# Optimization experiments

Hardware: AMD Instinct MI355X
Metric: run time of the kernel (lower is better)

## Reference

```python
import jax, jax.numpy as jnp
import numpy as np

C = 512
NUM_GROUPS = 32
EPS = 1e-6


def setup_inputs() -> dict:
    key = jax.random.key(0)
    ks = jax.random.split(key, 6)
    B, H, W = 4, 64, 64
    x = jax.random.normal(ks[0], (B, H, W, C), dtype=jnp.float32)
    # GroupNorm affine params (flax default init: scale=1, bias=0)
    gn_scale = jnp.ones((C,), jnp.float32)
    gn_bias = jnp.zeros((C,), jnp.float32)
    # 1x1 convs == per-pixel dense layers; weight [C_in, C_out], bias [C_out]
    def dense(k):
        return jax.random.normal(k, (C, C), dtype=jnp.float32) * 0.02
    wq, wk, wv, wo = dense(ks[1]), dense(ks[2]), dense(ks[3]), dense(ks[4])
    bq = jnp.zeros((C,), jnp.float32)
    bk = jnp.zeros((C,), jnp.float32)
    bv = jnp.zeros((C,), jnp.float32)
    bo = jnp.zeros((C,), jnp.float32)
    return {"x": x, "gn_scale": gn_scale, "gn_bias": gn_bias,
            "wq": wq, "bq": bq, "wk": wk, "bk": bk,
            "wv": wv, "bv": bv, "wo": wo, "bo": bo}


def _group_norm(x, scale, bias):
    B, H, W, Cc = x.shape
    g = NUM_GROUPS
    xg = x.reshape(B, H, W, g, Cc // g)
    mean = jnp.mean(xg, axis=(1, 2, 4), keepdims=True)
    var = jnp.var(xg, axis=(1, 2, 4), keepdims=True)
    xn = (xg - mean) * jax.lax.rsqrt(var + EPS)
    xn = xn.reshape(B, H, W, Cc)
    return xn * scale + bias


def reference(x, gn_scale, gn_bias, wq, bq, wk, bk, wv, bv, wo, bo):
    B, H, W, Cc = x.shape
    hn = _group_norm(x, gn_scale, gn_bias)
    # 1x1 convs
    q = (hn @ wq + bq).reshape(B, H * W, Cc)
    k = (hn @ wk + bk).reshape(B, H * W, Cc)
    v = (hn @ wv + bv).reshape(B, H * W, Cc)
    scale = jnp.asarray(Cc, x.dtype) ** -0.5
    # scores[b,i,j] = <q_i, k_j> * c^-0.5; softmax over keys j
    attn = jax.nn.softmax(jnp.einsum('bic,bjc->bij', q, k) * scale, axis=-1)
    out = jnp.einsum('bij,bjc->bic', attn, v).reshape(B, H, W, Cc)
    return x + (out @ wo + bo)
```

## Files before the change

kernel.cpp:

```cpp
#include <hip/hip_runtime.h>


typedef __attribute__((ext_vector_type(8))) __bf16 bf16x8;
typedef __attribute__((ext_vector_type(4))) __bf16 bf16x4;
typedef __attribute__((ext_vector_type(4))) float  floatx4;

#define C_DIM 512
#define SPB   4096
#define MTOT  16384

#define HN_OFF  ((size_t)0)
#define Q_OFF   ((size_t)16 << 20)
#define K_OFF   ((size_t)32 << 20)
#define V4_OFF  ((size_t)48 << 20)
#define WT_OFF  ((size_t)64 << 20)
#define O1_OFF  ((size_t)68 << 20)
#define ML_OFF  ((size_t)84 << 20)
#define GS_OFF  (ML_OFF + (size_t)(256 << 10))

__device__ inline floatx4 mfma16(bf16x8 a, bf16x8 b, floatx4 c) {
    return __builtin_amdgcn_mfma_f32_16x16x32_bf16(a, b, c, 0, 0, 0);
}

__device__ inline void gload16(const void* g, void* lds) {
    __builtin_amdgcn_global_load_lds(
        (const __attribute__((address_space(1))) unsigned int*)g,
        (__attribute__((address_space(3))) unsigned int*)lds, 16, 0, 0);
}

__global__ __launch_bounds__(256) void zero_stats(float* gstats) {
    gstats[threadIdx.x] = 0.f;
}

__global__ __launch_bounds__(256) void gn_stats(
    const float* __restrict__ x, float* __restrict__ gstats) {
    int bg = blockIdx.x;
    int b = bg >> 5, g = bg & 31;
    int tid = threadIdx.x;
    int cq = tid & 3, s0 = tid >> 2;
    const float* base = x + (size_t)b * SPB * C_DIM + g * 16 + cq * 4
                          + (size_t)blockIdx.y * 1024 * C_DIM;
    float sum = 0.f, sq = 0.f;
#pragma unroll 4
    for (int i = 0; i < 16; ++i) {
        floatx4 v = *(const floatx4*)(base + (size_t)(i * 64 + s0) * C_DIM);
        sum += v[0] + v[1] + v[2] + v[3];
        sq  += v[0]*v[0] + v[1]*v[1] + v[2]*v[2] + v[3]*v[3];
    }
#pragma unroll
    for (int off = 1; off < 64; off <<= 1) {
        sum += __shfl_xor(sum, off);
        sq  += __shfl_xor(sq,  off);
    }
    __shared__ float sm[8];
    int w = tid >> 6, lane = tid & 63;
    if (lane == 0) { sm[w] = sum; sm[4 + w] = sq; }
    __syncthreads();
    if (tid == 0) {
        atomicAdd(&gstats[bg * 2],     sm[0] + sm[1] + sm[2] + sm[3]);
        atomicAdd(&gstats[bg * 2 + 1], sm[4] + sm[5] + sm[6] + sm[7]);
    }
}

__global__ __launch_bounds__(256) void gn_apply(
    const float* __restrict__ x, const float* __restrict__ gstats,
    const float* __restrict__ gsc, const float* __restrict__ gbi,
    __bf16* __restrict__ hn) {
    int bg = blockIdx.x;
    int b = bg >> 5, g = bg & 31;
    int tid = threadIdx.x;
    int cq = tid & 3, s0 = tid >> 2;
    float S  = gstats[bg * 2], Qs = gstats[bg * 2 + 1];
    float mean = S * (1.f / 65536.f);
    float var  = Qs * (1.f / 65536.f) - mean * mean;
    float rstd = rsqrtf(var + 1e-6f);
    float sc[4], bi[4];
#pragma unroll
    for (int j = 0; j < 4; ++j) {
        float s_ = gsc[g * 16 + cq * 4 + j] * rstd;
        sc[j] = s_;
        bi[j] = gbi[g * 16 + cq * 4 + j] - mean * s_;
    }
    size_t off = (size_t)b * SPB * C_DIM + g * 16 + cq * 4
               + (size_t)blockIdx.y * 1024 * C_DIM;
    const float* base = x + off;
    __bf16* hbase = hn + off;
#pragma unroll 4
    for (int i = 0; i < 16; ++i) {
        floatx4 v = *(const floatx4*)(base + (size_t)(i * 64 + s0) * C_DIM);
        bf16x4 o;
#pragma unroll
        for (int j = 0; j < 4; ++j) o[j] = (__bf16)(v[j] * sc[j] + bi[j]);
        *(bf16x4*)(hbase + (size_t)(i * 64 + s0) * C_DIM) = o;
    }
}

__global__ __launch_bounds__(256) void wt_kernel(
    const float* __restrict__ w0, const float* __restrict__ w1,
    const float* __restrict__ w2, const float* __restrict__ w3,
    __bf16* __restrict__ wt) {
    const float* srcs[4] = {w0, w1, w2, w3};
    const float* src = srcs[blockIdx.z];
    __bf16* dst = wt + (size_t)blockIdx.z * C_DIM * C_DIM;
    __shared__ float tile[32][33];
    int tx = threadIdx.x & 31, ty = threadIdx.x >> 5;
    int gx = blockIdx.x * 32, gy = blockIdx.y * 32;
#pragma unroll
    for (int i = 0; i < 4; ++i)
        tile[ty + i * 8][tx] = src[(size_t)(gy + ty + i * 8) * C_DIM + gx + tx];
    __syncthreads();
#pragma unroll
    for (int i = 0; i < 4; ++i) {
        int n = gx + ty + i * 8;
        int k = gy + tx;
        dst[(size_t)n * C_DIM + k] = (__bf16)tile[tx][ty + i * 8];
    }
}

__global__ __launch_bounds__(256, 2) void proj_qkv(
    const __bf16* __restrict__ hn, const __bf16* __restrict__ wt_all,
    const float* __restrict__ bq, const float* __restrict__ bk,
    const float* __restrict__ bv, __bf16* __restrict__ qout,
    __bf16* __restrict__ kout, __bf16* __restrict__ v4out) {
    int z = blockIdx.z;
    const __bf16* wt = wt_all + (size_t)z * C_DIM * C_DIM;
    const float* bias = (z == 0) ? bq : (z == 1) ? bk : bv;
    __shared__ __bf16 Alds[128 * 32];
    __shared__ __bf16 Blds[128 * 32];
    int tid = threadIdx.x, lane = tid & 63, w = tid >> 6;
    int c = lane & 15, quad = lane >> 4;
    int wm = w & 1, wn = w >> 1;
    int mbase = blockIdx.x * 128, nbase = blockIdx.y * 128;
    floatx4 acc[4][4] = {};
    for (int kb = 0; kb < 16; ++kb) {
        __syncthreads();
#pragma unroll
        for (int p = 0; p < 2; ++p) {
            int chunk0 = w * 128 + p * 64;
            int chunk = chunk0 + lane;
            int row = chunk >> 2, qk = chunk & 3;
            gload16(hn + (size_t)(mbase + row) * C_DIM + kb * 32 + qk * 8, Alds + chunk0 * 8);
            gload16(wt + (size_t)(nbase + row) * C_DIM + kb * 32 + qk * 8, Blds + chunk0 * 8);
        }
        __syncthreads();
        bf16x8 af[4], bfr[4];
#pragma unroll
        for (int mt = 0; mt < 4; ++mt)
            af[mt] = *(const bf16x8*)(Alds + (wm * 64 + mt * 16 + c) * 32 + quad * 8);
#pragma unroll
        for (int nt = 0; nt < 4; ++nt)
            bfr[nt] = *(const bf16x8*)(Blds + (wn * 64 + nt * 16 + c) * 32 + quad * 8);
#pragma unroll
        for (int mt = 0; mt < 4; ++mt)
#pragma unroll
            for (int nt = 0; nt < 4; ++nt)
                acc[mt][nt] = mfma16(af[mt], bfr[nt], acc[mt][nt]);
    }
    float scale = (z == 0) ? 0.0441941738241592f : 1.0f;
#pragma unroll
    for (int nt = 0; nt < 4; ++nt) {
        int n = nbase + wn * 64 + nt * 16 + c;
        float bval = bias[n];
#pragma unroll
        for (int mt = 0; mt < 4; ++mt) {
            int m0 = mbase + wm * 64 + mt * 16 + quad * 4;
#pragma unroll
            for (int r = 0; r < 4; ++r) {
                int m = m0 + r;
                float val = (acc[mt][nt][r] + bval) * scale;
                if (z == 0)      qout[(size_t)m * C_DIM + n] = (__bf16)val;
                else if (z == 1) kout[(size_t)m * C_DIM + n] = (__bf16)val;
                else {
                    int bb = m >> 12, pos = m & 4095;
                    v4out[((size_t)(bb * 512 + (pos >> 3)) * C_DIM + n) * 8 + (pos & 7)] = (__bf16)val;
                }
            }
        }
    }
}

__device__ inline void stage_K(const __bf16* kbase, int key0,
                               __bf16* Klds, int w, int lane) {
#pragma unroll
    for (int p = 0; p < 8; ++p) {
        int chunk0 = w * 512 + p * 64;
        int chunk = chunk0 + lane;
        gload16(kbase + (size_t)(key0 + (chunk & 31)) * C_DIM + (chunk >> 5) * 8,
                Klds + chunk0 * 8);
    }
}

__global__ __launch_bounds__(256, 2) void flash_kernel(
    const __bf16* __restrict__ q, const __bf16* __restrict__ kmat,
    const __bf16* __restrict__ v4, __bf16* __restrict__ op0,
    __bf16* __restrict__ op1, float* __restrict__ lpart) {
    __shared__ __bf16 Klds[16384];
    __shared__ __bf16 Plds[64 * 40];
    int tid = threadIdx.x, lane = tid & 63, w = tid >> 6;
    int c = lane & 15, quad = lane >> 4;
    int bid = blockIdx.x;
    int xcd = bid & 7;
    int b = xcd >> 1, h = xcd & 1, qt = bid >> 3;

    const __bf16* qp = q + ((size_t)(b * SPB + qt * 64 + w * 16 + c)) * C_DIM + quad * 8;
    bf16x8 qf[16];
#pragma unroll
    for (int ks = 0; ks < 16; ++ks) qf[ks] = *(const bf16x8*)(qp + ks * 32);
    floatx4 o[4][8];
#pragma unroll
    for (int mg = 0; mg < 4; ++mg)
#pragma unroll
        for (int t = 0; t < 8; ++t) o[mg][t] = (floatx4){0.f, 0.f, 0.f, 0.f};
    float l_r[4] = {0.f, 0.f, 0.f, 0.f};

    const __bf16* kbase = kmat + (size_t)b * SPB * C_DIM;
    const __bf16* vbase = v4 + (size_t)b * 512 * C_DIM * 8;

    stage_K(kbase, h * 2048, Klds, w, lane);
    __syncthreads();

    for (int kt = 0; kt < 64; ++kt) {
        int key0 = h * 2048 + kt * 32;
        const __bf16* vp = vbase
            + ((size_t)((key0 >> 3) + quad) * C_DIM + w * 128 + c) * 8;
        bf16x8 vreg[8];
#pragma unroll
        for (int t = 0; t < 8; ++t)
            vreg[t] = *(const bf16x8*)(vp + (size_t)t * 16 * 8);
        floatx4 s0 = (floatx4){0.f,0.f,0.f,0.f}, s1 = (floatx4){0.f,0.f,0.f,0.f};
#pragma unroll
        for (int ks = 0; ks < 16; ++ks) {
            bf16x8 k0 = *(const bf16x8*)(Klds + (((ks * 4 + quad) * 32) + c) * 8);
            bf16x8 k1 = *(const bf16x8*)(Klds + (((ks * 4 + quad) * 32) + c + 16) * 8);
            s0 = mfma16(qf[ks], k0, s0);
            s1 = mfma16(qf[ks], k1, s1);
        }
#pragma unroll
        for (int r = 0; r < 4; ++r) {
            float p0 = __expf(s0[r]);
            float p1 = __expf(s1[r]);
            l_r[r] += p0 + p1;
            int row = w * 16 + quad * 4 + r;
            Plds[row * 40 + c]      = (__bf16)p0;
            Plds[row * 40 + c + 16] = (__bf16)p1;
        }
        __syncthreads();
        int kn = (kt < 63) ? kt + 1 : 63;
        stage_K(kbase, h * 2048 + kn * 32, Klds, w, lane);
        bf16x8 pf[4];
#pragma unroll
        for (int mg = 0; mg < 4; ++mg)
            pf[mg] = *(const bf16x8*)(Plds + (mg * 16 + c) * 40 + quad * 8);
#pragma unroll
        for (int t = 0; t < 8; ++t) {
#pragma unroll
            for (int mg = 0; mg < 4; ++mg)
                o[mg][t] = mfma16(pf[mg], vreg[t], o[mg][t]);
        }
        __syncthreads();
    }
#pragma unroll
    for (int r = 0; r < 4; ++r) {
        float l = l_r[r];
        l += __shfl_xor(l, 1);
        l += __shfl_xor(l, 2);
        l += __shfl_xor(l, 4);
        l += __shfl_xor(l, 8);
        l_r[r] = l;
    }
    if (c == 0) {
#pragma unroll
        for (int r = 0; r < 4; ++r) {
            int grow = b * SPB + qt * 64 + w * 16 + quad * 4 + r;
            lpart[h * MTOT + grow] = l_r[r];
        }
    }
    __bf16* ob = h ? op1 : op0;
#pragma unroll
    for (int mg = 0; mg < 4; ++mg)
#pragma unroll
        for (int t = 0; t < 8; ++t)
#pragma unroll
            for (int r = 0; r < 4; ++r) {
                int grow = b * SPB + qt * 64 + mg * 16 + quad * 4 + r;
                ob[(size_t)grow * C_DIM + w * 128 + t * 16 + c] = (__bf16)o[mg][t][r];
            }
}

__global__ __launch_bounds__(256) void combine_kernel(
    const __bf16* __restrict__ o0, const __bf16* __restrict__ o1,
    const float* __restrict__ lpart, __bf16* __restrict__ attn) {
    int tid = threadIdx.x, lane = tid & 63, w = tid >> 6;
    int rbase = blockIdx.x * 64 + w * 16;
    for (int rr = 0; rr < 16; ++rr) {
        int row = rbase + rr;
        float inv = 1.f / (lpart[row] + lpart[MTOT + row]);
        bf16x8 v0 = *(const bf16x8*)(o0 + (size_t)row * C_DIM + lane * 8);
        bf16x8 v1 = *(const bf16x8*)(o1 + (size_t)row * C_DIM + lane * 8);
        bf16x8 r;
#pragma unroll
        for (int j = 0; j < 8; ++j) r[j] = (__bf16)(((float)v0[j] + (float)v1[j]) * inv);
        *(bf16x8*)(attn + (size_t)row * C_DIM + lane * 8) = r;
    }
}

__global__ __launch_bounds__(256, 2) void proj_out(
    const __bf16* __restrict__ attn, const __bf16* __restrict__ wot,
    const float* __restrict__ bo, const float* __restrict__ x,
    float* __restrict__ out) {
    __shared__ __bf16 Alds[128 * 32];
    __shared__ __bf16 Blds[128 * 32];
    int tid = threadIdx.x, lane = tid & 63, w = tid >> 6;
    int c = lane & 15, quad = lane >> 4;
    int wm = w & 1, wn = w >> 1;
    int mbase = blockIdx.x * 128, nbase = blockIdx.y * 128;
    floatx4 acc[4][4] = {};
    for (int kb = 0; kb < 16; ++kb) {
        __syncthreads();
#pragma unroll
        for (int p = 0; p < 2; ++p) {
            int chunk0 = w * 128 + p * 64;
            int chunk = chunk0 + lane;
            int row = chunk >> 2, qk = chunk & 3;
            gload16(attn + (size_t)(mbase + row) * C_DIM + kb * 32 + qk * 8, Alds + chunk0 * 8);
            gload16(wot + (size_t)(nbase + row) * C_DIM + kb * 32 + qk * 8, Blds + chunk0 * 8);
        }
        __syncthreads();
        bf16x8 af[4], bfr[4];
#pragma unroll
        for (int mt = 0; mt < 4; ++mt)
            af[mt] = *(const bf16x8*)(Alds + (wm * 64 + mt * 16 + c) * 32 + quad * 8);
#pragma unroll
        for (int nt = 0; nt < 4; ++nt)
            bfr[nt] = *(const bf16x8*)(Blds + (wn * 64 + nt * 16 + c) * 32 + quad * 8);
#pragma unroll
        for (int mt = 0; mt < 4; ++mt)
#pragma unroll
            for (int nt = 0; nt < 4; ++nt)
                acc[mt][nt] = mfma16(af[mt], bfr[nt], acc[mt][nt]);
    }
#pragma unroll
    for (int nt = 0; nt < 4; ++nt) {
        int n = nbase + wn * 64 + nt * 16 + c;
        float bval = bo[n];
#pragma unroll
        for (int mt = 0; mt < 4; ++mt) {
            int m0 = mbase + wm * 64 + mt * 16 + quad * 4;
#pragma unroll
            for (int r = 0; r < 4; ++r) {
                size_t idx = (size_t)(m0 + r) * C_DIM + n;
                out[idx] = acc[mt][nt][r] + bval + x[idx];
            }
        }
    }
}

extern "C" void kernel_launch(void* const* d_in, const int* in_sizes, int n_in,
                              void* d_out, int out_size, void* d_ws, size_t ws_size,
                              hipStream_t stream) {
    const float* x   = (const float*)d_in[0];
    const float* gsc = (const float*)d_in[1];
    const float* gbi = (const float*)d_in[2];
    const float* wq  = (const float*)d_in[3];
    const float* bq  = (const float*)d_in[4];
    const float* wk  = (const float*)d_in[5];
    const float* bk  = (const float*)d_in[6];
    const float* wv  = (const float*)d_in[7];
    const float* bv  = (const float*)d_in[8];
    const float* wo  = (const float*)d_in[9];
    const float* bo  = (const float*)d_in[10];
    char* ws = (char*)d_ws;
    __bf16* hn  = (__bf16*)(ws + HN_OFF);
    __bf16* qb  = (__bf16*)(ws + Q_OFF);
    __bf16* kb  = (__bf16*)(ws + K_OFF);
    __bf16* v4  = (__bf16*)(ws + V4_OFF);
    __bf16* wt  = (__bf16*)(ws + WT_OFF);
    __bf16* op0 = (__bf16*)(ws + HN_OFF);
    __bf16* op1 = (__bf16*)(ws + O1_OFF);
    float*  lp  = (float*)(ws + ML_OFF);
    float*  gs  = (float*)(ws + GS_OFF);
    __bf16* attn = qb;
    float* out = (float*)d_out;

    zero_stats<<<1, 256, 0, stream>>>(gs);
    wt_kernel<<<dim3(16, 16, 4), 256, 0, stream>>>(wq, wk, wv, wo, wt);
    gn_stats<<<dim3(128, 4), 256, 0, stream>>>(x, gs);
    gn_apply<<<dim3(128, 4), 256, 0, stream>>>(x, gs, gsc, gbi, hn);
    proj_qkv<<<dim3(128, 4, 3), 256, 0, stream>>>(hn, wt, bq, bk, bv, qb, kb, v4);
    flash_kernel<<<512, 256, 0, stream>>>(qb, kb, v4, op0, op1, lp);
    combine_kernel<<<256, 256, 0, stream>>>(op0, op1, lp, attn);
    proj_out<<<dim3(128, 4), 256, 0, stream>>>(attn, wt + (size_t)3 * C_DIM * C_DIM, bo, x, out);
}
```

Before: 472.4 us.

## Split attention keys four ways when workspace allows, with four-way combine

Templates the flash kernel on the number of key splits and, when the workspace is large enough, launches 1024 blocks that each cover a quarter of the keys instead of 512 blocks covering half. The combine kernel sums four partial outputs and four denominators. The launch bound is raised from 2 to 4 blocks per CU to increase occupancy. The aim is more parallelism on the 256-CU device. In exchange it writes and reads twice as many bf16 partial outputs, and the tighter register budget could cause spills given the large o/qf register arrays.

```diff
diff --git a/kernel.cpp b/kernel.cpp
--- a/kernel.cpp
+++ b/kernel.cpp
@@ -17,6 +17,11 @@
 #define O1_OFF  ((size_t)68 << 20)
 #define ML_OFF  ((size_t)84 << 20)
 #define GS_OFF  (ML_OFF + (size_t)(256 << 10))
+#define O2_OFF  ((size_t)84 << 20)
+#define O3_OFF  ((size_t)100 << 20)
+#define ML4_OFF ((size_t)116 << 20)
+#define GS4_OFF (ML4_OFF + (size_t)(256 << 10))
+#define NEED4   (GS4_OFF + (size_t)(64 << 10))
 
 __device__ inline floatx4 mfma16(bf16x8 a, bf16x8 b, floatx4 c) {
     return __builtin_amdgcn_mfma_f32_16x16x32_bf16(a, b, c, 0, 0, 0);
@@ -190,17 +195,28 @@
     }
 }
 
-__global__ __launch_bounds__(256, 2) void flash_kernel(
+template <int NS>
+__global__ __launch_bounds__(256, 4) void flash_kernel(
     const __bf16* __restrict__ q, const __bf16* __restrict__ kmat,
     const __bf16* __restrict__ v4, __bf16* __restrict__ op0,
-    __bf16* __restrict__ op1, float* __restrict__ lpart) {
+    __bf16* __restrict__ op1, __bf16* __restrict__ op2,
+    __bf16* __restrict__ op3, float* __restrict__ lpart) {
     __shared__ __bf16 Klds[16384];
     __shared__ __bf16 Plds[64 * 40];
     int tid = threadIdx.x, lane = tid & 63, w = tid >> 6;
     int c = lane & 15, quad = lane >> 4;
     int bid = blockIdx.x;
-    int xcd = bid & 7;
-    int b = xcd >> 1, h = xcd & 1, qt = bid >> 3;
+    int b, h, qt;
+    if constexpr (NS == 2) {
+        int xcd = bid & 7;
+        b = xcd >> 1; h = xcd & 1; qt = bid >> 3;
+    } else {
+        int x = bid & 7, i = bid >> 3;
+        int g = x + 8 * (i & 1);
+        b = g >> 2; h = g & 3; qt = i >> 1;
+    }
+    constexpr int KPS = 4096 / NS;
+    constexpr int NIT = KPS / 32;
 
     const __bf16* qp = q + ((size_t)(b * SPB + qt * 64 + w * 16 + c)) * C_DIM + quad * 8;
     bf16x8 qf[16];
@@ -216,11 +232,11 @@
     const __bf16* kbase = kmat + (size_t)b * SPB * C_DIM;
     const __bf16* vbase = v4 + (size_t)b * 512 * C_DIM * 8;
 
-    stage_K(kbase, h * 2048, Klds, w, lane);
+    stage_K(kbase, h * KPS, Klds, w, lane);
     __syncthreads();
 
-    for (int kt = 0; kt < 64; ++kt) {
-        int key0 = h * 2048 + kt * 32;
+    for (int kt = 0; kt < NIT; ++kt) {
+        int key0 = h * KPS + kt * 32;
         const __bf16* vp = vbase
             + ((size_t)((key0 >> 3) + quad) * C_DIM + w * 128 + c) * 8;
         bf16x8 vreg[8];
@@ -245,8 +261,8 @@
             Plds[row * 40 + c + 16] = (__bf16)p1;
         }
         __syncthreads();
-        int kn = (kt < 63) ? kt + 1 : 63;
-        stage_K(kbase, h * 2048 + kn * 32, Klds, w, lane);
+        int kn = (kt < NIT - 1) ? kt + 1 : NIT - 1;
+        stage_K(kbase, h * KPS + kn * 32, Klds, w, lane);
         bf16x8 pf[4];
 #pragma unroll
         for (int mg = 0; mg < 4; ++mg)
@@ -275,7 +291,9 @@
             lpart[h * MTOT + grow] = l_r[r];
         }
     }
-    __bf16* ob = h ? op1 : op0;
+    __bf16* ob;
+    if constexpr (NS == 2) ob = h ? op1 : op0;
+    else ob = (h == 0) ? op0 : (h == 1) ? op1 : (h == 2) ? op2 : op3;
 #pragma unroll
     for (int mg = 0; mg < 4; ++mg)
 #pragma unroll
@@ -287,19 +305,34 @@
             }
 }
 
+template <int NS>
 __global__ __launch_bounds__(256) void combine_kernel(
     const __bf16* __restrict__ o0, const __bf16* __restrict__ o1,
+    const __bf16* __restrict__ o2, const __bf16* __restrict__ o3,
     const float* __restrict__ lpart, __bf16* __restrict__ attn) {
     int tid = threadIdx.x, lane = tid & 63, w = tid >> 6;
     int rbase = blockIdx.x * 64 + w * 16;
     for (int rr = 0; rr < 16; ++rr) {
         int row = rbase + rr;
-        float inv = 1.f / (lpart[row] + lpart[MTOT + row]);
+        float lsum = lpart[row] + lpart[MTOT + row];
+        if constexpr (NS == 4)
+            lsum += lpart[2 * MTOT + row] + lpart[3 * MTOT + row];
+        float inv = 1.f / lsum;
         bf16x8 v0 = *(const bf16x8*)(o0 + (size_t)row * C_DIM + lane * 8);
         bf16x8 v1 = *(const bf16x8*)(o1 + (size_t)row * C_DIM + lane * 8);
         bf16x8 r;
-#pragma unroll
-        for (int j = 0; j < 8; ++j) r[j] = (__bf16)(((float)v0[j] + (float)v1[j]) * inv);
+        if constexpr (NS == 4) {
+            bf16x8 v2 = *(const bf16x8*)(o2 + (size_t)row * C_DIM + lane * 8);
+            bf16x8 v3 = *(const bf16x8*)(o3 + (size_t)row * C_DIM + lane * 8);
+#pragma unroll
+            for (int j = 0; j < 8; ++j)
+                r[j] = (__bf16)((((float)v0[j] + (float)v1[j]) +
+                                 ((float)v2[j] + (float)v3[j])) * inv);
+        } else {
+#pragma unroll
+            for (int j = 0; j < 8; ++j)
+                r[j] = (__bf16)(((float)v0[j] + (float)v1[j]) * inv);
+        }
         *(bf16x8*)(attn + (size_t)row * C_DIM + lane * 8) = r;
     }
 }
@@ -377,17 +410,26 @@
     __bf16* wt  = (__bf16*)(ws + WT_OFF);
     __bf16* op0 = (__bf16*)(ws + HN_OFF);
     __bf16* op1 = (__bf16*)(ws + O1_OFF);
-    float*  lp  = (float*)(ws + ML_OFF);
-    float*  gs  = (float*)(ws + GS_OFF);
     __bf16* attn = qb;
     float* out = (float*)d_out;
+
+    bool use4 = (ws_size >= NEED4);
+    __bf16* op2 = use4 ? (__bf16*)(ws + O2_OFF) : op0;
+    __bf16* op3 = use4 ? (__bf16*)(ws + O3_OFF) : op1;
+    float*  lp  = use4 ? (float*)(ws + ML4_OFF) : (float*)(ws + ML_OFF);
+    float*  gs  = use4 ? (float*)(ws + GS4_OFF) : (float*)(ws + GS_OFF);
 
     zero_stats<<<1, 256, 0, stream>>>(gs);
     wt_kernel<<<dim3(16, 16, 4), 256, 0, stream>>>(wq, wk, wv, wo, wt);
     gn_stats<<<dim3(128, 4), 256, 0, stream>>>(x, gs);
     gn_apply<<<dim3(128, 4), 256, 0, stream>>>(x, gs, gsc, gbi, hn);
     proj_qkv<<<dim3(128, 4, 3), 256, 0, stream>>>(hn, wt, bq, bk, bv, qb, kb, v4);
-    flash_kernel<<<512, 256, 0, stream>>>(qb, kb, v4, op0, op1, lp);
-    combine_kernel<<<256, 256, 0, stream>>>(op0, op1, lp, attn);
+    if (use4) {
+        flash_kernel<4><<<1024, 256, 0, stream>>>(qb, kb, v4, op0, op1, op2, op3, lp);
+        combine_kernel<4><<<256, 256, 0, stream>>>(op0, op1, op2, op3, lp, attn);
+    } else {
+        flash_kernel<2><<<512, 256, 0, stream>>>(qb, kb, v4, op0, op1, op2, op3, lp);
+        combine_kernel<2><<<256, 256, 0, stream>>>(op0, op1, op2, op3, lp, attn);
+    }
     proj_out<<<dim3(128, 4), 256, 0, stream>>>(attn, wt + (size_t)3 * C_DIM * C_DIM, bo, x, out);
 }
```

After: 1.312 ms. +177.7%, slower.
